# Performance work log

Measured on AMD Instinct MI355X. Metric: run time of the kernel, lower is better.

The kernel has to match this reference:

```python
import jax, jax.numpy as jnp
import numpy as np
from jax import lax

_CONV_SHAPES = [(384, 3), (384, 384), (768, 384), (768, 768), (1536, 768), (512, 1536)]
_BN_CH = [384, 384, 768, 768, 1536, 512, 1024, 1024]
_LIN_SHAPES = [(1024, 8192), (1024, 1024), (10, 1024)]
_BATCH = 32
_EPS = 1e-5


def _sign_ste(t):
    # deterministic binarization with straight-through gradient (identity)
    return t + lax.stop_gradient(jnp.sign(t) - t)


def _conv(x, w, b):
    y = lax.conv_general_dilated(x, w, (1, 1), 'SAME',
                                 dimension_numbers=('NCHW', 'OIHW', 'NCHW'))
    return y + b[None, :, None, None]


def _pool(x):
    return lax.reduce_window(x, -jnp.inf, lax.max, (1, 1, 2, 2), (1, 1, 2, 2), 'VALID')


def _bn2d(x, g, b, m, v):
    inv = g / jnp.sqrt(v + _EPS)
    return (x - m[None, :, None, None]) * inv[None, :, None, None] + b[None, :, None, None]


def _bn1d(x, g, b, m, v):
    return (x - m) * (g / jnp.sqrt(v + _EPS)) + b


def _ht(x):
    return jnp.clip(x, -1.0, 1.0)


def _apply(x, cw, cb, g, b, m, v, m9, v9, lw, lb):
    h = _conv(x, _sign_ste(cw[0]), cb[0])  # first conv: real-valued (3-channel) input
    h = _ht(_bn2d(h, g[0], b[0], m[0], v[0]))
    h = _pool(_conv(_sign_ste(h), _sign_ste(cw[1]), cb[1]))
    h = _ht(_bn2d(h, g[1], b[1], m[1], v[1]))
    h = _conv(_sign_ste(h), _sign_ste(cw[2]), cb[2])
    h = _ht(_bn2d(h, g[2], b[2], m[2], v[2]))
    h = _pool(_conv(_sign_ste(h), _sign_ste(cw[3]), cb[3]))
    h = _ht(_bn2d(h, g[3], b[3], m[3], v[3]))
    h = _conv(_sign_ste(h), _sign_ste(cw[4]), cb[4])
    h = _ht(_bn2d(h, g[4], b[4], m[4], v[4]))
    h = _pool(_conv(_sign_ste(h), _sign_ste(cw[5]), cb[5]))
    h = _ht(_bn2d(h, g[5], b[5], m[5], v[5]))
    h = h.reshape(-1, 512 * 4 * 4)
    h = _sign_ste(h) @ _sign_ste(lw[0]).T + lb[0]
    h = _ht(_bn1d(h, g[6], b[6], m[6], v[6]))
    h = _sign_ste(h) @ _sign_ste(lw[1]).T + lb[1]
    h = _ht(_bn1d(h, g[7], b[7], m[7], v[7]))
    h = _sign_ste(h) @ _sign_ste(lw[2]).T + lb[2]
    h = (h - m9) / jnp.sqrt(v9 + _EPS)  # BatchNorm1d(num_classes, affine=False)
    return jax.nn.log_softmax(h, axis=-1)


def setup_inputs() -> dict:
    keys = iter(jax.random.split(jax.random.key(0), 128))
    inp = {'x': jax.random.normal(next(keys), (_BATCH, 3, 32, 32), jnp.float32)}
    for i, (o, c) in enumerate(_CONV_SHAPES, 1):
        inp[f'cw{i}'] = jax.random.normal(next(keys), (o, c, 3, 3), jnp.float32) * 0.05
        inp[f'cb{i}'] = jax.random.normal(next(keys), (o,), jnp.float32) * 0.05
    for i, c in enumerate(_BN_CH, 1):
        inp[f'g{i}'] = jnp.ones((c,), jnp.float32)
        inp[f'b{i}'] = jnp.zeros((c,), jnp.float32)
        inp[f'm{i}'] = jax.random.normal(next(keys), (c,), jnp.float32) * 0.1
        inp[f'v{i}'] = jax.random.uniform(next(keys), (c,), jnp.float32) + 0.5
    inp['m9'] = jax.random.normal(next(keys), (10,), jnp.float32) * 0.1
    inp['v9'] = jax.random.uniform(next(keys), (10,), jnp.float32) + 0.5
    for i, (o, c) in enumerate(_LIN_SHAPES, 1):
        inp[f'lw{i}'] = jax.random.normal(next(keys), (o, c), jnp.float32) * 0.05
        inp[f'lb{i}'] = jax.random.normal(next(keys), (o,), jnp.float32) * 0.05
    return inp


def reference(x, cw1, cb1, cw2, cb2, cw3, cb3, cw4, cb4, cw5, cb5, cw6, cb6,
              g1, b1, m1, v1, g2, b2, m2, v2, g3, b3, m3, v3, g4, b4, m4, v4,
              g5, b5, m5, v5, g6, b6, m6, v6, g7, b7, m7, v7, g8, b8, m8, v8,
              m9, v9, lw1, lb1, lw2, lb2, lw3, lb3):
    cw = [cw1, cw2, cw3, cw4, cw5, cw6]
    cb = [cb1, cb2, cb3, cb4, cb5, cb6]
    g = [g1, g2, g3, g4, g5, g6, g7, g8]
    b = [b1, b2, b3, b4, b5, b6, b7, b8]
    m = [m1, m2, m3, m4, m5, m6, m7, m8]
    v = [v1, v2, v3, v4, v5, v6, v7, v8]
    lw = [lw1, lw2, lw3]
    lb = [lb1, lb2, lb3]
    return _apply(x, cw, cb, g, b, m, v, m9, v9, lw, lb)
```

## Files before the change

### kernel.cpp

```cpp
#include <hip/hip_runtime.h>
#include <hip/hip_bf16.h>
#include <math.h>

typedef unsigned long long ull;

#define EPS 1e-5

__global__ __launch_bounds__(256) void pack_conv_w(const float* __restrict__ w,
                                                   ull* __restrict__ out,
                                                   int Cout, int Cin) {
    extern __shared__ float lw[];
    int co = blockIdx.x;
    int n = Cin * 9;
    const float* base = w + (size_t)co * n;
    for (int i = threadIdx.x; i < n; i += 256) lw[i] = base[i];
    __syncthreads();
    int KC = Cin >> 6;
    int lane = threadIdx.x & 63;
    int wv = threadIdx.x >> 6;
    for (int widx = wv; widx < 9 * KC; widx += 4) {
        int tap = widx / KC, kc = widx % KC;
        float f = lw[(kc * 64 + lane) * 9 + tap];
        ull bits = __ballot(f > 0.f);
        if (lane == 0) out[((size_t)tap * KC + kc) * Cout + co] = bits;
    }
}

__global__ __launch_bounds__(256) void pack_lw1(const float* __restrict__ w,
                                                ull* __restrict__ out) {
    __shared__ float lw[512 * 17];
    int co = blockIdx.x;
    const float* base = w + (size_t)co * 8192;
    for (int k = threadIdx.x; k < 8192; k += 256)
        lw[(k >> 4) * 17 + (k & 15)] = base[k];
    __syncthreads();
    int lane = threadIdx.x & 63;
    int wv = threadIdx.x >> 6;
    for (int wi = wv; wi < 128; wi += 4) {
        int s = wi >> 3, kc = wi & 7;
        float f = lw[(kc * 64 + lane) * 17 + s];
        ull bits = __ballot(f > 0.f);
        if (lane == 0) out[(size_t)wi * 1024 + co] = bits;
    }
}

__global__ __launch_bounds__(256) void pack_lw_lin(const float* __restrict__ w,
                                                   ull* __restrict__ out,
                                                   int rows) {
    __shared__ float lw[1024];
    int co = blockIdx.x;
    const float* base = w + (size_t)co * 1024;
    for (int k = threadIdx.x; k < 1024; k += 256) lw[k] = base[k];
    __syncthreads();
    int lane = threadIdx.x & 63;
    int wv = threadIdx.x >> 6;
    for (int wi = wv; wi < 16; wi += 4) {
        float f = lw[wi * 64 + lane];
        ull bits = __ballot(f > 0.f);
        if (lane == 0) out[(size_t)wi * rows + co] = bits;
    }
}

__global__ __launch_bounds__(384) void conv1_bn_sign(
    const float* __restrict__ x, const float* __restrict__ cw,
    const float* __restrict__ cb, const float* __restrict__ g,
    const float* __restrict__ bb, const float* __restrict__ m,
    const float* __restrict__ v, ull* __restrict__ out) {
    __shared__ double xs[3][3][34];
    int blk = blockIdx.x;
    int y = blk & 31, n = blk >> 5;
    for (int i = threadIdx.x; i < 3 * 3 * 34; i += 384) {
        int col = i % 34;
        int r = i / 34;
        int ky = r % 3, ci = r / 3;
        int iy = y + ky - 1, ix = col - 1;
        double vv = 0.0;
        if ((unsigned)iy < 32u && (unsigned)ix < 32u)
            vv = (double)x[(((size_t)n * 3 + ci) * 32 + iy) * 32 + ix];
        xs[ci][ky][col] = vv;
    }
    __syncthreads();
    int co = threadIdx.x;
    double ws[27];
#pragma unroll
    for (int q = 0; q < 27; ++q) {
        float wv = cw[(size_t)co * 27 + q];
        ws[q] = (wv > 0.f) ? 1.0 : ((wv < 0.f) ? -1.0 : 0.0);
    }
    double inv = (double)g[co] / sqrt((double)v[co] + EPS);
    double addc = (double)cb[co] - (double)m[co];
    double bbv = (double)bb[co];
    ull* op = out + (size_t)blk * 32 * 6 + (co >> 6);
    for (int xx = 0; xx < 32; ++xx) {
        double acc = 0.0;
#pragma unroll
        for (int ci = 0; ci < 3; ++ci)
#pragma unroll
            for (int ky = 0; ky < 3; ++ky)
#pragma unroll
                for (int kx = 0; kx < 3; ++kx)
                    acc = fma(ws[(ci * 3 + ky) * 3 + kx], xs[ci][ky][xx + kx], acc);
        double tt = (acc + addc) * inv + bbv;
        ull mask = __ballot(tt > 0.0);
        if ((threadIdx.x & 63) == 0) op[(size_t)xx * 6] = mask;
    }
}

template <int KC, int KCC, int POOL, int PB, int BLK>
__global__ __launch_bounds__(BLK, 4) void binconv_kernel(
    const ull* __restrict__ act, const ull* __restrict__ wgt,
    const float* __restrict__ cb, const float* __restrict__ g,
    const float* __restrict__ bb, const float* __restrict__ m,
    const float* __restrict__ v, ull* __restrict__ out,
    int Hin, int Win, int Cout) {
    const int Hout = Hin / POOL, Wout = Win / POOL;
    constexpr int WH = POOL + 2, WW = PB * POOL + 2;
    constexpr int NPIX = PB * POOL * POOL;
    constexpr int NCH = KC / KCC;
    __shared__ __align__(16) ull lact[NCH][WH * WW][KCC];
    int xb = blockIdx.x % (Wout / PB);
    int t = blockIdx.x / (Wout / PB);
    int yo = t % Hout;
    int n = t / Hout;
    int xo0 = xb * PB;
    int iy0 = yo * POOL - 1, ix0 = xo0 * POOL - 1;

    for (int i = threadIdx.x; i < WH * WW * KC; i += BLK) {
        int kc = i % KC;
        int pp = i / KC;
        int wy = pp / WW, wx = pp % WW;
        int iy = iy0 + wy, ix = ix0 + wx;
        ull val = 0;
        if ((unsigned)iy < (unsigned)Hin && (unsigned)ix < (unsigned)Win)
            val = act[(((size_t)n * Hin + iy) * Win + ix) * KC + kc];
        lact[kc / KCC][pp][kc % KCC] = val;
    }
    __syncthreads();

    int co = blockIdx.y * BLK + (int)threadIdx.x;

    int tot[NPIX];
#pragma unroll
    for (int i = 0; i < NPIX; ++i) tot[i] = 0;

#pragma unroll 1
    for (int ch = 0; ch < NCH; ++ch) {
        const int kc0 = ch * KCC;
        ull w[9][KCC];
#pragma unroll
        for (int tap = 0; tap < 9; ++tap)
#pragma unroll
            for (int i = 0; i < KCC; ++i)
                w[tap][i] = wgt[((size_t)tap * KC + kc0 + i) * Cout + co];

#pragma unroll
        for (int r = 0; r < WH; ++r) {
            if ((unsigned)(iy0 + r) >= (unsigned)Hin) continue;
#pragma unroll
            for (int c = 0; c < WW; ++c) {
                if ((unsigned)(ix0 + c) >= (unsigned)Win) continue;
                const ull* lp = lact[ch][r * WW + c];
                ull a[KCC];
#pragma unroll
                for (int i = 0; i < KCC; ++i) a[i] = lp[i];
#pragma unroll
                for (int dy = (r >= 2 ? r - 2 : 0);
                     dy <= (r < POOL - 1 ? r : POOL - 1); ++dy) {
                    const int ky = r - dy;
#pragma unroll
                    for (int j = (c >= 2 ? c - 2 : 0);
                         j <= (c < PB * POOL - 1 ? c : PB * POOL - 1); ++j) {
                        const int kx = c - j;
                        const int tap = ky * 3 + kx;
                        const int pix =
                            (j / POOL) * (POOL * POOL) + dy * POOL + (j % POOL);
#pragma unroll
                        for (int i = 0; i < KCC; ++i)
                            tot[pix] += __popcll(a[i] ^ w[tap][i]);
                    }
                }
            }
        }
    }

    double inv = (double)g[co] / sqrt((double)v[co] + EPS);
    double addc = (double)cb[co] - (double)m[co];
    double bbv = (double)bb[co];

    int KCOUT = Cout >> 6;
#pragma unroll
    for (int px = 0; px < PB; ++px) {
        int best = 0x80000000;
#pragma unroll
        for (int dy = 0; dy < POOL; ++dy)
#pragma unroll
            for (int dx = 0; dx < POOL; ++dx) {
                int py = yo * POOL + dy;
                int pxa = (xo0 + px) * POOL + dx;
                int cy = 3 - (py == 0) - (py == Hin - 1);
                int cx = 3 - (pxa == 0) - (pxa == Win - 1);
                int dot = cy * cx * (KC * 64) -
                          2 * tot[px * POOL * POOL + dy * POOL + dx];
                best = max(best, dot);
            }
        double tt = ((double)best + addc) * inv + bbv;
        ull mask = __ballot(tt > 0.0);
        if ((threadIdx.x & 63) == 0)
            out[(size_t)((n * Hout + yo) * Wout + xo0 + px) * KCOUT + (co >> 6)] =
                mask;
    }
}

template <int KCIN>
__global__ __launch_bounds__(256) void binfc_kernel(
    const ull* __restrict__ act, const ull* __restrict__ wgt,
    const float* __restrict__ lb, const float* __restrict__ g,
    const float* __restrict__ bb, const float* __restrict__ m,
    const float* __restrict__ v, ull* __restrict__ out, int Cout) {
    int n = blockIdx.x;
    int co = blockIdx.y * 256 + (int)threadIdx.x;
    const ull* ap = act + (size_t)n * KCIN;
    int mism = 0;
#pragma unroll 8
    for (int kc = 0; kc < KCIN; ++kc)
        mism += __popcll(ap[kc] ^ wgt[(size_t)kc * Cout + co]);
    int dot = 64 * KCIN - 2 * mism;
    double tt = ((double)dot + (double)lb[co] - (double)m[co]) *
                    ((double)g[co] / sqrt((double)v[co] + EPS)) +
                (double)bb[co];
    ull mask = __ballot(tt > 0.0);
    if (((int)threadIdx.x & 63) == 0)
        out[(size_t)n * (Cout >> 6) + ((unsigned)co >> 6)] = mask;
}

__global__ __launch_bounds__(64) void fc3_softmax(
    const ull* __restrict__ act, const ull* __restrict__ wgt,
    const float* __restrict__ lb, const float* __restrict__ m9,
    const float* __restrict__ v9, float* __restrict__ out) {
    int n = blockIdx.x;
    __shared__ double z[10];
    int j = threadIdx.x;
    if (j < 10) {
        const ull* ap = act + (size_t)n * 16;
        int mism = 0;
#pragma unroll
        for (int kc = 0; kc < 16; ++kc) mism += __popcll(ap[kc] ^ wgt[kc * 10 + j]);
        int dot = 1024 - 2 * mism;
        z[j] = ((double)dot + (double)lb[j] - (double)m9[j]) /
               sqrt((double)v9[j] + EPS);
    }
    __syncthreads();
    if (j < 10) {
        double mx = z[0];
        for (int k = 1; k < 10; ++k) mx = fmax(mx, z[k]);
        double s = 0.0;
        for (int k = 0; k < 10; ++k) s += exp(z[k] - mx);
        out[n * 10 + j] = (float)(z[j] - mx - log(s));
    }
}

extern "C" void kernel_launch(void* const* d_in, const int* in_sizes, int n_in,
                              void* d_out, int out_size, void* d_ws, size_t ws_size,
                              hipStream_t stream) {
    (void)in_sizes; (void)n_in; (void)out_size; (void)ws_size;

    const float* x   = (const float*)d_in[0];
    const float* cw[6], *cbv[6];
    for (int i = 0; i < 6; ++i) {
        cw[i]  = (const float*)d_in[1 + 2 * i];
        cbv[i] = (const float*)d_in[2 + 2 * i];
    }
    const float *G[8], *B[8], *M[8], *V[8];
    for (int i = 0; i < 8; ++i) {
        G[i] = (const float*)d_in[13 + 4 * i];
        B[i] = (const float*)d_in[14 + 4 * i];
        M[i] = (const float*)d_in[15 + 4 * i];
        V[i] = (const float*)d_in[16 + 4 * i];
    }
    const float* m9  = (const float*)d_in[45];
    const float* v9  = (const float*)d_in[46];
    const float* lw1 = (const float*)d_in[47];
    const float* lb1 = (const float*)d_in[48];
    const float* lw2 = (const float*)d_in[49];
    const float* lb2 = (const float*)d_in[50];
    const float* lw3 = (const float*)d_in[51];
    const float* lb3 = (const float*)d_in[52];
    float* outp = (float*)d_out;

    ull* ws = (ull*)d_ws;
    ull* W2  = ws + 0;
    ull* W3  = ws + 20736;
    ull* W4  = ws + 62208;
    ull* W5  = ws + 145152;
    ull* W6  = ws + 311040;
    ull* FW1 = ws + 421632;
    ull* FW2 = ws + 552704;
    ull* FW3 = ws + 569088;
    ull* A1  = ws + 569248;
    ull* A2  = ws + 765856;
    ull* A3  = ws + 815008;
    ull* A4  = ws + 913312;
    ull* A5  = ws + 937888;
    ull* A6  = ws + 987040;
    ull* F1  = ws + 991136;
    ull* F2  = ws + 991648;

    pack_conv_w<<<384, 256, 384 * 9 * 4, stream>>>(cw[1], W2, 384, 384);
    pack_conv_w<<<768, 256, 384 * 9 * 4, stream>>>(cw[2], W3, 768, 384);
    pack_conv_w<<<768, 256, 768 * 9 * 4, stream>>>(cw[3], W4, 768, 768);
    pack_conv_w<<<1536, 256, 768 * 9 * 4, stream>>>(cw[4], W5, 1536, 768);
    pack_conv_w<<<512, 256, 1536 * 9 * 4, stream>>>(cw[5], W6, 512, 1536);
    pack_lw1<<<1024, 256, 0, stream>>>(lw1, FW1);
    pack_lw_lin<<<1024, 256, 0, stream>>>(lw2, FW2, 1024);
    pack_lw_lin<<<10, 256, 0, stream>>>(lw3, FW3, 10);

    conv1_bn_sign<<<32 * 32, 384, 0, stream>>>(x, cw[0], cbv[0], G[0], B[0],
                                               M[0], V[0], A1);
    binconv_kernel<6, 3, 2, 4, 192><<<dim3(2048, 2), 192, 0, stream>>>(
        A1, W2, cbv[1], G[1], B[1], M[1], V[1], A2, 32, 32, 384);
    binconv_kernel<6, 3, 1, 8, 256><<<dim3(1024, 3), 256, 0, stream>>>(
        A2, W3, cbv[2], G[2], B[2], M[2], V[2], A3, 16, 16, 768);
    binconv_kernel<12, 4, 2, 4, 256><<<dim3(512, 3), 256, 0, stream>>>(
        A3, W4, cbv[3], G[3], B[3], M[3], V[3], A4, 16, 16, 768);
    binconv_kernel<12, 4, 1, 8, 256><<<dim3(256, 6), 256, 0, stream>>>(
        A4, W5, cbv[4], G[4], B[4], M[4], V[4], A5, 8, 8, 1536);
    binconv_kernel<24, 4, 2, 4, 256><<<dim3(128, 2), 256, 0, stream>>>(
        A5, W6, cbv[5], G[5], B[5], M[5], V[5], A6, 8, 8, 512);
    binfc_kernel<128><<<dim3(32, 4), 256, 0, stream>>>(A6, FW1, lb1, G[6], B[6],
                                                       M[6], V[6], F1, 1024);
    binfc_kernel<16><<<dim3(32, 4), 256, 0, stream>>>(F1, FW2, lb2, G[7], B[7],
                                                      M[7], V[7], F2, 1024);
    fc3_softmax<<<32, 64, 0, stream>>>(F2, FW3, lb3, m9, v9, outp);
}
```

Baseline: 700.2 us.

## Remove border branches from binary conv loop and correct padding afterward

The binconv inner loop no longer skips out-of-bounds rows and columns. Padding is zero in shared memory, and XOR with zero counts the weight's set bits, so a post-pass on border blocks subtracts the per-tap weight popcounts. This makes the unrolled loop branch-free. The same change flattens the shared-memory layout, lowers the occupancy hint in launch_bounds from 4 to 3, and sets KCC to 3 for the deeper layers. The price is extra global weight reads and popcounts in border blocks, plus a register and occupancy trade-off.

After: 786.3 us. 12.3% more time.

```diff
diff --git a/kernel.cpp b/kernel.cpp
--- a/kernel.cpp
+++ b/kernel.cpp
@@ -107,7 +107,7 @@
 }
 
 template <int KC, int KCC, int POOL, int PB, int BLK>
-__global__ __launch_bounds__(BLK, 4) void binconv_kernel(
+__global__ __launch_bounds__(BLK, 3) void binconv_kernel(
     const ull* __restrict__ act, const ull* __restrict__ wgt,
     const float* __restrict__ cb, const float* __restrict__ g,
     const float* __restrict__ bb, const float* __restrict__ m,
@@ -117,7 +117,7 @@
     constexpr int WH = POOL + 2, WW = PB * POOL + 2;
     constexpr int NPIX = PB * POOL * POOL;
     constexpr int NCH = KC / KCC;
-    __shared__ __align__(16) ull lact[NCH][WH * WW][KCC];
+    __shared__ __align__(16) ull lact[WH * WW * KC];
     int xb = blockIdx.x % (Wout / PB);
     int t = blockIdx.x / (Wout / PB);
     int yo = t % Hout;
@@ -126,14 +126,13 @@
     int iy0 = yo * POOL - 1, ix0 = xo0 * POOL - 1;
 
     for (int i = threadIdx.x; i < WH * WW * KC; i += BLK) {
-        int kc = i % KC;
         int pp = i / KC;
         int wy = pp / WW, wx = pp % WW;
         int iy = iy0 + wy, ix = ix0 + wx;
         ull val = 0;
         if ((unsigned)iy < (unsigned)Hin && (unsigned)ix < (unsigned)Win)
-            val = act[(((size_t)n * Hin + iy) * Win + ix) * KC + kc];
-        lact[kc / KCC][pp][kc % KCC] = val;
+            val = act[(((size_t)n * Hin + iy) * Win + ix) * KC + (i % KC)];
+        lact[i] = val;
     }
     __syncthreads();
 
@@ -154,12 +153,10 @@
                 w[tap][i] = wgt[((size_t)tap * KC + kc0 + i) * Cout + co];
 
 #pragma unroll
-        for (int r = 0; r < WH; ++r) {
-            if ((unsigned)(iy0 + r) >= (unsigned)Hin) continue;
+        for (int r = 0; r < WH; ++r)
 #pragma unroll
             for (int c = 0; c < WW; ++c) {
-                if ((unsigned)(ix0 + c) >= (unsigned)Win) continue;
-                const ull* lp = lact[ch][r * WW + c];
+                const ull* lp = lact + ((size_t)r * WW + c) * KC + kc0;
                 ull a[KCC];
 #pragma unroll
                 for (int i = 0; i < KCC; ++i) a[i] = lp[i];
@@ -180,7 +177,36 @@
                     }
                 }
             }
+    }
+
+    if (iy0 < 0 || iy0 + WH > Hin || ix0 < 0 || ix0 + WW > Win) {
+        int pw[9];
+#pragma unroll
+        for (int tap = 0; tap < 9; ++tap) {
+            int s = 0;
+#pragma unroll 1
+            for (int kc = 0; kc < KC; ++kc)
+                s += __popcll(wgt[((size_t)tap * KC + kc) * Cout + co]);
+            pw[tap] = s;
         }
+#pragma unroll
+        for (int px = 0; px < PB; ++px)
+#pragma unroll
+            for (int dy = 0; dy < POOL; ++dy)
+#pragma unroll
+                for (int dx = 0; dx < POOL; ++dx) {
+                    int py = yo * POOL + dy;
+                    int pxa = (xo0 + px) * POOL + dx;
+                    int pix = px * (POOL * POOL) + dy * POOL + dx;
+#pragma unroll
+                    for (int ky = 0; ky < 3; ++ky)
+#pragma unroll
+                        for (int kx = 0; kx < 3; ++kx) {
+                            if ((unsigned)(py + ky - 1) >= (unsigned)Hin ||
+                                (unsigned)(pxa + kx - 1) >= (unsigned)Win)
+                                tot[pix] -= pw[ky * 3 + kx];
+                        }
+                }
     }
 
     double inv = (double)g[co] / sqrt((double)v[co] + EPS);
@@ -320,11 +346,11 @@
         A1, W2, cbv[1], G[1], B[1], M[1], V[1], A2, 32, 32, 384);
     binconv_kernel<6, 3, 1, 8, 256><<<dim3(1024, 3), 256, 0, stream>>>(
         A2, W3, cbv[2], G[2], B[2], M[2], V[2], A3, 16, 16, 768);
-    binconv_kernel<12, 4, 2, 4, 256><<<dim3(512, 3), 256, 0, stream>>>(
+    binconv_kernel<12, 3, 2, 4, 256><<<dim3(512, 3), 256, 0, stream>>>(
         A3, W4, cbv[3], G[3], B[3], M[3], V[3], A4, 16, 16, 768);
-    binconv_kernel<12, 4, 1, 8, 256><<<dim3(256, 6), 256, 0, stream>>>(
+    binconv_kernel<12, 3, 1, 8, 256><<<dim3(256, 6), 256, 0, stream>>>(
         A4, W5, cbv[4], G[4], B[4], M[4], V[4], A5, 8, 8, 1536);
-    binconv_kernel<24, 4, 2, 4, 256><<<dim3(128, 2), 256, 0, stream>>>(
+    binconv_kernel<24, 3, 2, 4, 256><<<dim3(128, 2), 256, 0, stream>>>(
         A5, W6, cbv[5], G[5], B[5], M[5], V[5], A6, 8, 8, 512);
     binfc_kernel<128><<<dim3(32, 4), 256, 0, stream>>>(A6, FW1, lb1, G[6], B[6],
                                                        M[6], V[6], F1, 1024);
```

## Read binary conv activations directly from global memory instead of LDS staging

Applied to the files above, without the earlier changes.

Removes the shared-memory staging of the input activation window and the block barrier in the binary conv kernel. Each thread now loads the activation row words straight from global memory, which is uniform across the block and so acts as a broadcast through the cache. The channel loop now steps one 64-bit word at a time, and the spatial dimensions and Cout become template constants. The occupancy hint rises from 4 to 6. This trades LDS traffic and the barrier for more redundant global and cache loads per thread, along with less work per loop iteration.

Result: no change. 699.2 us (-0.1%).

```diff
diff --git a/kernel.cpp b/kernel.cpp
--- a/kernel.cpp
+++ b/kernel.cpp
@@ -106,36 +106,24 @@
     }
 }
 
-template <int KC, int KCC, int POOL, int PB, int BLK>
-__global__ __launch_bounds__(BLK, 4) void binconv_kernel(
+template <int KC, int POOL, int PB, int BLK, int HIN, int WIN, int COUT>
+__global__ __launch_bounds__(BLK, 6) void binconv_kernel(
     const ull* __restrict__ act, const ull* __restrict__ wgt,
     const float* __restrict__ cb, const float* __restrict__ g,
     const float* __restrict__ bb, const float* __restrict__ m,
-    const float* __restrict__ v, ull* __restrict__ out,
-    int Hin, int Win, int Cout) {
-    const int Hout = Hin / POOL, Wout = Win / POOL;
+    const float* __restrict__ v, ull* __restrict__ out) {
+    constexpr int HOUT = HIN / POOL, WOUT = WIN / POOL;
     constexpr int WH = POOL + 2, WW = PB * POOL + 2;
     constexpr int NPIX = PB * POOL * POOL;
-    constexpr int NCH = KC / KCC;
-    __shared__ __align__(16) ull lact[NCH][WH * WW][KCC];
-    int xb = blockIdx.x % (Wout / PB);
-    int t = blockIdx.x / (Wout / PB);
-    int yo = t % Hout;
-    int n = t / Hout;
+    constexpr int XB = WOUT / PB;
+    int xb = (int)blockIdx.x % XB;
+    int t = (int)blockIdx.x / XB;
+    int yo = t % HOUT;
+    int n = t / HOUT;
     int xo0 = xb * PB;
     int iy0 = yo * POOL - 1, ix0 = xo0 * POOL - 1;
-
-    for (int i = threadIdx.x; i < WH * WW * KC; i += BLK) {
-        int kc = i % KC;
-        int pp = i / KC;
-        int wy = pp / WW, wx = pp % WW;
-        int iy = iy0 + wy, ix = ix0 + wx;
-        ull val = 0;
-        if ((unsigned)iy < (unsigned)Hin && (unsigned)ix < (unsigned)Win)
-            val = act[(((size_t)n * Hin + iy) * Win + ix) * KC + kc];
-        lact[kc / KCC][pp][kc % KCC] = val;
-    }
-    __syncthreads();
+    const bool left = (ix0 >= 0);
+    const bool right = (ix0 + WW <= WIN);
 
     int co = blockIdx.y * BLK + (int)threadIdx.x;
 
@@ -144,25 +132,28 @@
     for (int i = 0; i < NPIX; ++i) tot[i] = 0;
 
 #pragma unroll 1
-    for (int ch = 0; ch < NCH; ++ch) {
-        const int kc0 = ch * KCC;
-        ull w[9][KCC];
+    for (int ch = 0; ch < KC; ++ch) {
+        ull w[9];
 #pragma unroll
         for (int tap = 0; tap < 9; ++tap)
-#pragma unroll
-            for (int i = 0; i < KCC; ++i)
-                w[tap][i] = wgt[((size_t)tap * KC + kc0 + i) * Cout + co];
+            w[tap] = wgt[((size_t)tap * KC + ch) * COUT + co];
 
 #pragma unroll
         for (int r = 0; r < WH; ++r) {
-            if ((unsigned)(iy0 + r) >= (unsigned)Hin) continue;
+            int iy = iy0 + r;
+            if ((unsigned)iy >= (unsigned)HIN) continue;
+            const ull* bp =
+                act + (((size_t)n * HIN + iy) * WIN + ix0) * KC + ch;
+            ull a[WW];
+            a[0] = left ? bp[0] : 0;
+#pragma unroll
+            for (int c = 1; c < WW - 1; ++c) a[c] = bp[(size_t)c * KC];
+            a[WW - 1] = right ? bp[(size_t)(WW - 1) * KC] : 0;
+
 #pragma unroll
             for (int c = 0; c < WW; ++c) {
-                if ((unsigned)(ix0 + c) >= (unsigned)Win) continue;
-                const ull* lp = lact[ch][r * WW + c];
-                ull a[KCC];
-#pragma unroll
-                for (int i = 0; i < KCC; ++i) a[i] = lp[i];
+                if (c == 0 && !left) continue;
+                if (c == WW - 1 && !right) continue;
 #pragma unroll
                 for (int dy = (r >= 2 ? r - 2 : 0);
                      dy <= (r < POOL - 1 ? r : POOL - 1); ++dy) {
@@ -174,9 +165,7 @@
                         const int tap = ky * 3 + kx;
                         const int pix =
                             (j / POOL) * (POOL * POOL) + dy * POOL + (j % POOL);
-#pragma unroll
-                        for (int i = 0; i < KCC; ++i)
-                            tot[pix] += __popcll(a[i] ^ w[tap][i]);
+                        tot[pix] += __popcll(a[c] ^ w[tap]);
                     }
                 }
             }
@@ -187,7 +176,7 @@
     double addc = (double)cb[co] - (double)m[co];
     double bbv = (double)bb[co];
 
-    int KCOUT = Cout >> 6;
+    constexpr int KCOUT = COUT >> 6;
 #pragma unroll
     for (int px = 0; px < PB; ++px) {
         int best = 0x80000000;
@@ -197,8 +186,8 @@
             for (int dx = 0; dx < POOL; ++dx) {
                 int py = yo * POOL + dy;
                 int pxa = (xo0 + px) * POOL + dx;
-                int cy = 3 - (py == 0) - (py == Hin - 1);
-                int cx = 3 - (pxa == 0) - (pxa == Win - 1);
+                int cy = 3 - (py == 0) - (py == HIN - 1);
+                int cx = 3 - (pxa == 0) - (pxa == WIN - 1);
                 int dot = cy * cx * (KC * 64) -
                           2 * tot[px * POOL * POOL + dy * POOL + dx];
                 best = max(best, dot);
@@ -206,7 +195,7 @@
         double tt = ((double)best + addc) * inv + bbv;
         ull mask = __ballot(tt > 0.0);
         if ((threadIdx.x & 63) == 0)
-            out[(size_t)((n * Hout + yo) * Wout + xo0 + px) * KCOUT + (co >> 6)] =
+            out[(size_t)((n * HOUT + yo) * WOUT + xo0 + px) * KCOUT + (co >> 6)] =
                 mask;
     }
 }
@@ -316,16 +305,16 @@
 
     conv1_bn_sign<<<32 * 32, 384, 0, stream>>>(x, cw[0], cbv[0], G[0], B[0],
                                                M[0], V[0], A1);
-    binconv_kernel<6, 3, 2, 4, 192><<<dim3(2048, 2), 192, 0, stream>>>(
-        A1, W2, cbv[1], G[1], B[1], M[1], V[1], A2, 32, 32, 384);
-    binconv_kernel<6, 3, 1, 8, 256><<<dim3(1024, 3), 256, 0, stream>>>(
-        A2, W3, cbv[2], G[2], B[2], M[2], V[2], A3, 16, 16, 768);
-    binconv_kernel<12, 4, 2, 4, 256><<<dim3(512, 3), 256, 0, stream>>>(
-        A3, W4, cbv[3], G[3], B[3], M[3], V[3], A4, 16, 16, 768);
-    binconv_kernel<12, 4, 1, 8, 256><<<dim3(256, 6), 256, 0, stream>>>(
-        A4, W5, cbv[4], G[4], B[4], M[4], V[4], A5, 8, 8, 1536);
-    binconv_kernel<24, 4, 2, 4, 256><<<dim3(128, 2), 256, 0, stream>>>(
-        A5, W6, cbv[5], G[5], B[5], M[5], V[5], A6, 8, 8, 512);
+    binconv_kernel<6, 2, 4, 192, 32, 32, 384><<<dim3(2048, 2), 192, 0, stream>>>(
+        A1, W2, cbv[1], G[1], B[1], M[1], V[1], A2);
+    binconv_kernel<6, 1, 8, 256, 16, 16, 768><<<dim3(1024, 3), 256, 0, stream>>>(
+        A2, W3, cbv[2], G[2], B[2], M[2], V[2], A3);
+    binconv_kernel<12, 2, 4, 256, 16, 16, 768><<<dim3(512, 3), 256, 0, stream>>>(
+        A3, W4, cbv[3], G[3], B[3], M[3], V[3], A4);
+    binconv_kernel<12, 1, 8, 256, 8, 8, 1536><<<dim3(256, 6), 256, 0, stream>>>(
+        A4, W5, cbv[4], G[4], B[4], M[4], V[4], A5);
+    binconv_kernel<24, 2, 4, 256, 8, 8, 512><<<dim3(128, 2), 256, 0, stream>>>(
+        A5, W6, cbv[5], G[5], B[5], M[5], V[5], A6);
     binfc_kernel<128><<<dim3(32, 4), 256, 0, stream>>>(A6, FW1, lb1, G[6], B[6],
                                                        M[6], V[6], F1, 1024);
     binfc_kernel<16><<<dim3(32, 4), 256, 0, stream>>>(F1, FW2, lb2, G[7], B[7],
```
